# Optimization experiments

Measured on AMD Instinct MI355X. Metric: run time of the kernel, lower is better.

## Reference

```python
import jax, jax.numpy as jnp
import numpy as np

EPS = 1e-9


def _resolve(circle_pos, circle_radius, aabb_pos, aabb_half):
    Nc = circle_pos.shape[0]
    Na = aabb_pos.shape[0]

    # ---- circle vs circle: push apart along center-to-center normal ----
    d = circle_pos[:, None, :] - circle_pos[None, :, :]          # [Nc,Nc,2]
    d2 = jnp.sum(d * d, axis=-1)                                 # [Nc,Nc]
    off_diag = ~jnp.eye(Nc, dtype=bool)
    dist = jnp.sqrt(jnp.where(d2 > EPS, d2, 1.0))
    pen = circle_radius[:, None] + circle_radius[None, :] - dist
    hit = off_diag & (d2 > EPS) & (pen > 0)
    normal = d / dist[..., None]
    # each body moves half the penetration toward itself; summing over the
    # full (symmetric) matrix resolves every unordered pair exactly once
    corr_cc = jnp.sum(jnp.where(hit[..., None], 0.5 * pen[..., None] * normal, 0.0), axis=1)

    # ---- aabb vs aabb: push along minimum-overlap axis ----
    da = aabb_pos[:, None, :] - aabb_pos[None, :, :]             # [Na,Na,2]
    ov = aabb_half[:, None, :] + aabb_half[None, :, :] - jnp.abs(da)
    hit_a = (~jnp.eye(Na, dtype=bool)) & (ov[..., 0] > 0) & (ov[..., 1] > 0)
    sgn = jnp.where(da >= 0, 1.0, -1.0)
    use_x = ov[..., 0] <= ov[..., 1]
    zeros = jnp.zeros_like(ov[..., 0])
    push_x = jnp.stack([0.5 * ov[..., 0] * sgn[..., 0], zeros], axis=-1)
    push_y = jnp.stack([zeros, 0.5 * ov[..., 1] * sgn[..., 1]], axis=-1)
    push = jnp.where(use_x[..., None], push_x, push_y)
    corr_aa = jnp.sum(jnp.where(hit_a[..., None], push, 0.0), axis=1)

    # ---- circle vs aabb: closest point on box ----
    rel = circle_pos[:, None, :] - aabb_pos[None, :, :]          # [Nc,Na,2]
    closest = jnp.clip(rel, -aabb_half[None, :, :], aabb_half[None, :, :])
    diff = rel - closest
    dd2 = jnp.sum(diff * diff, axis=-1)
    ddist = jnp.sqrt(jnp.where(dd2 > EPS, dd2, 1.0))
    pen_ca = circle_radius[:, None] - ddist
    hit_ca = (dd2 > EPS) & (pen_ca > 0)
    n_ca = diff / ddist[..., None]
    push_ca = jnp.where(hit_ca[..., None], 0.5 * pen_ca[..., None] * n_ca, 0.0)
    corr_c = jnp.sum(push_ca, axis=1)     # on circles
    corr_a = -jnp.sum(push_ca, axis=0)    # equal-and-opposite on boxes

    new_circle = circle_pos + corr_cc + corr_c
    new_aabb = aabb_pos + corr_aa + corr_a
    return jnp.concatenate([new_circle, new_aabb], axis=0)   # [Nc+Na, 2]


def setup_inputs() -> dict:
    key = jax.random.key(0)
    k1, k2, k3, k4 = jax.random.split(key, 4)
    circle_pos = jax.random.normal(k1, (4096, 2), dtype=jnp.float32)
    circle_radius = jax.random.uniform(k2, (4096,), dtype=jnp.float32)
    aabb_pos = jax.random.normal(k3, (2048, 2), dtype=jnp.float32)
    aabb_half = jax.random.uniform(k4, (2048, 2), dtype=jnp.float32)
    return {"circle_pos": circle_pos, "circle_radius": circle_radius,
            "aabb_pos": aabb_pos, "aabb_half": aabb_half}


def reference(circle_pos, circle_radius, aabb_pos, aabb_half):
    return _resolve(circle_pos, circle_radius, aabb_pos, aabb_half)
```

## Files before the change

kernel.cpp:

```cpp
#include <hip/hip_runtime.h>
#include <math.h>

#define EPS 1e-9f

__global__ void prep(const float2* __restrict__ cpos,
                     const float*  __restrict__ crad,
                     const float2* __restrict__ apos,
                     const float2* __restrict__ ahalf,
                     float4* __restrict__ P,
                     float2* __restrict__ out,
                     int Nc, int Ntot) {
    int i = blockIdx.x * blockDim.x + threadIdx.x;
    if (i >= Ntot) return;
    if (i < Nc) {
        const float2 p = cpos[i];
        P[i]   = make_float4(p.x, p.y, crad[i], 0.0f);
        out[i] = p;
    } else {
        const float2 a = apos[i - Nc];
        const float2 h = ahalf[i - Nc];
        P[i]   = make_float4(a.x, a.y, h.x, h.y);
        out[i] = a;
    }
}

__global__ __launch_bounds__(256)
void collide(const float4* __restrict__ P,
             float* __restrict__ out,
             int Nc, int Ntot) {
    const int lane  = threadIdx.x & 63;
    const int w     = __builtin_amdgcn_readfirstlane(threadIdx.x >> 6);
    const int i     = (blockIdx.x << 6) + lane;
    const int jbase = (blockIdx.y * 4 + w) << 6;

    const float4 me = P[i];
    float ax = 0.0f, ay = 0.0f;

    const bool body_circle = ((int)(blockIdx.x << 6)) < Nc;
    const bool part_circle = (jbase < Nc);

    if (body_circle) {
        const float px = me.x, py = me.y, ri = me.z;
        if (part_circle) {
            #pragma unroll 8
            for (int k = 0; k < 64; ++k) {
                const float4 q = P[jbase + k];
                const float dx = px - q.x, dy = py - q.y;
                const float d2 = fmaf(dx, dx, dy * dy);
                const float r  = __builtin_amdgcn_rsqf(d2);
                const float pen = (ri + q.z) - d2 * r;
                const float s = (d2 > EPS && pen > 0.0f) ? 0.5f * pen * r : 0.0f;
                ax = fmaf(s, dx, ax);
                ay = fmaf(s, dy, ay);
            }
        } else {
            #pragma unroll 8
            for (int k = 0; k < 64; ++k) {
                const float4 q = P[jbase + k];
                const float rx = px - q.x, ry = py - q.y;
                const float cx = fminf(fmaxf(rx, -q.z), q.z);
                const float cy = fminf(fmaxf(ry, -q.w), q.w);
                const float dx = rx - cx, dy = ry - cy;
                const float d2 = fmaf(dx, dx, dy * dy);
                const float r  = __builtin_amdgcn_rsqf(d2);
                const float pen = ri - d2 * r;
                const float s = (d2 > EPS && pen > 0.0f) ? 0.5f * pen * r : 0.0f;
                ax = fmaf(s, dx, ax);
                ay = fmaf(s, dy, ay);
            }
        }
    } else {
        const float bx = me.x, by = me.y, hx = me.z, hy = me.w;
        if (part_circle) {
            #pragma unroll 8
            for (int k = 0; k < 64; ++k) {
                const float4 q = P[jbase + k];
                const float rx = q.x - bx, ry = q.y - by;
                const float cx = fminf(fmaxf(rx, -hx), hx);
                const float cy = fminf(fmaxf(ry, -hy), hy);
                const float dx = rx - cx, dy = ry - cy;
                const float d2 = fmaf(dx, dx, dy * dy);
                const float r  = __builtin_amdgcn_rsqf(d2);
                const float pen = q.z - d2 * r;
                const float s = (d2 > EPS && pen > 0.0f) ? -0.5f * pen * r : 0.0f;
                ax = fmaf(s, dx, ax);
                ay = fmaf(s, dy, ay);
            }
        } else {
            #pragma unroll 8
            for (int k = 0; k < 64; ++k) {
                const int j = jbase + k;
                const float4 q = P[j];
                const float dax = bx - q.x, day = by - q.y;
                const float ovx = hx + q.z - fabsf(dax);
                const float ovy = hy + q.w - fabsf(day);
                const bool hit = (j != i) && (ovx > 0.0f) && (ovy > 0.0f);
                const bool ux  = ovx <= ovy;
                ax += (hit && ux)  ? 0.5f * ovx * (dax >= 0.0f ? 1.0f : -1.0f) : 0.0f;
                ay += (hit && !ux) ? 0.5f * ovy * (day >= 0.0f ? 1.0f : -1.0f) : 0.0f;
            }
        }
    }

    __shared__ float sax[4][64];
    __shared__ float say[4][64];
    sax[w][lane] = ax;
    say[w][lane] = ay;
    __syncthreads();
    if (w == 0) {
        const float tx = sax[0][lane] + sax[1][lane] + sax[2][lane] + sax[3][lane];
        const float ty = say[0][lane] + say[1][lane] + say[2][lane] + say[3][lane];
        atomicAdd(&out[2 * i],     tx);
        atomicAdd(&out[2 * i + 1], ty);
    }
}

extern "C" void kernel_launch(void* const* d_in, const int* in_sizes, int n_in,
                              void* d_out, int out_size, void* d_ws, size_t ws_size,
                              hipStream_t stream) {
    (void)n_in; (void)out_size; (void)ws_size;

    const float2* cpos  = (const float2*)d_in[0];
    const float*  crad  = (const float*) d_in[1];
    const float2* apos  = (const float2*)d_in[2];
    const float2* ahalf = (const float2*)d_in[3];

    const int Nc   = in_sizes[1];
    const int Na   = in_sizes[2] / 2;
    const int Ntot = Nc + Na;

    float4* P = (float4*)d_ws;

    prep<<<(Ntot + 255) / 256, 256, 0, stream>>>(cpos, crad, apos, ahalf,
                                                 P, (float2*)d_out, Nc, Ntot);

    const int gx = (Ntot + 63) / 64;
    const int gy = (Ntot + 255) / 256;
    dim3 grid(gx, gy, 1);
    collide<<<grid, 256, 0, stream>>>(P, (float*)d_out, Nc, Ntot);
}
```

Measured before the change: 78.18 us.

## Exploit pair symmetry: process upper-triangular tile pairs with equal-and-opposite forces

```diff
diff --git a/kernel.cpp b/kernel.cpp
--- a/kernel.cpp
+++ b/kernel.cpp
@@ -14,7 +14,7 @@
     if (i >= Ntot) return;
     if (i < Nc) {
         const float2 p = cpos[i];
-        P[i]   = make_float4(p.x, p.y, crad[i], 0.0f);
+        P[i]   = make_float4(p.x, p.y, 0.5f * crad[i], 0.0f);
         out[i] = p;
     } else {
         const float2 a = apos[i - Nc];
@@ -24,95 +24,128 @@
     }
 }
 
+__device__ __forceinline__ int tri_off(int I) { return I * (193 - I) / 2; }
+
 __global__ __launch_bounds__(256)
 void collide(const float4* __restrict__ P,
              float* __restrict__ out,
-             int Nc, int Ntot) {
-    const int lane  = threadIdx.x & 63;
-    const int w     = __builtin_amdgcn_readfirstlane(threadIdx.x >> 6);
-    const int i     = (blockIdx.x << 6) + lane;
-    const int jbase = (blockIdx.y * 4 + w) << 6;
+             int Nc) {
+    const int lane = threadIdx.x & 63;
+    const int w    = threadIdx.x >> 6;
+    const int t    = blockIdx.x * 4 + w;
 
-    const float4 me = P[i];
+    int I = (int)((193.0f - sqrtf((float)(37249 - 8 * t))) * 0.5f);
+    while (tri_off(I + 1) <= t) ++I;
+    while (tri_off(I) > t) --I;
+    const int J = I + (t - tri_off(I));
+
+    const int tileC  = Nc >> 6;
+    const bool bodyC = I < tileC;
+    const bool partC = J < tileC;
+
+    __shared__ float4 Jd[4][128];
+    __shared__ float  FJx[4][128];
+    __shared__ float  FJy[4][128];
+
+    {
+        const float4 q = P[(J << 6) + lane];
+        Jd[w][lane]       = q;
+        Jd[w][lane + 64]  = q;
+        FJx[w][lane]      = 0.0f;  FJx[w][lane + 64] = 0.0f;
+        FJy[w][lane]      = 0.0f;  FJy[w][lane + 64] = 0.0f;
+    }
+    __syncthreads();
+
+    const float4 me = P[(I << 6) + lane];
     float ax = 0.0f, ay = 0.0f;
 
-    const bool body_circle = ((int)(blockIdx.x << 6)) < Nc;
-    const bool part_circle = (jbase < Nc);
-
-    if (body_circle) {
-        const float px = me.x, py = me.y, ri = me.z;
-        if (part_circle) {
+    if (I != J) {
+        if (partC) {
+            const float px = me.x, py = me.y, rih = me.z;
             #pragma unroll 8
-            for (int k = 0; k < 64; ++k) {
-                const float4 q = P[jbase + k];
-                const float dx = px - q.x, dy = py - q.y;
+            for (int m = 0; m < 64; ++m) {
+                const int slot = lane + m;
+                const float4 q = Jd[w][slot];
+                const float dx = q.x - px, dy = q.y - py;
                 const float d2 = fmaf(dx, dx, dy * dy);
                 const float r  = __builtin_amdgcn_rsqf(d2);
-                const float pen = (ri + q.z) - d2 * r;
-                const float s = (d2 > EPS && pen > 0.0f) ? 0.5f * pen * r : 0.0f;
-                ax = fmaf(s, dx, ax);
-                ay = fmaf(s, dy, ay);
+                const float s  = fmaxf(fmaf(rih + q.z, r, -0.5f), 0.0f);
+                const float fJx = s * dx, fJy = s * dy;
+                ax -= fJx; ay -= fJy;
+                atomicAdd(&FJx[w][slot], fJx);
+                atomicAdd(&FJy[w][slot], fJy);
             }
-        } else {
+        } else if (bodyC) {
+            const float px = me.x, py = me.y, rih = me.z;
             #pragma unroll 8
-            for (int k = 0; k < 64; ++k) {
-                const float4 q = P[jbase + k];
-                const float rx = px - q.x, ry = py - q.y;
+            for (int m = 0; m < 64; ++m) {
+                const int slot = lane + m;
+                const float4 q = Jd[w][slot];
+                const float rx = q.x - px, ry = q.y - py;
                 const float cx = fminf(fmaxf(rx, -q.z), q.z);
                 const float cy = fminf(fmaxf(ry, -q.w), q.w);
                 const float dx = rx - cx, dy = ry - cy;
                 const float d2 = fmaf(dx, dx, dy * dy);
                 const float r  = __builtin_amdgcn_rsqf(d2);
-                const float pen = ri - d2 * r;
-                const float s = (d2 > EPS && pen > 0.0f) ? 0.5f * pen * r : 0.0f;
-                ax = fmaf(s, dx, ax);
-                ay = fmaf(s, dy, ay);
+                float s = fmaxf(fmaf(rih, r, -0.5f), 0.0f);
+                s = (d2 > EPS) ? s : 0.0f;
+                const float fJx = s * dx, fJy = s * dy;
+                ax -= fJx; ay -= fJy;
+                atomicAdd(&FJx[w][slot], fJx);
+                atomicAdd(&FJy[w][slot], fJy);
+            }
+        } else {
+            const float bx = me.x, by = me.y, hx = me.z, hy = me.w;
+            #pragma unroll 8
+            for (int m = 0; m < 64; ++m) {
+                const int slot = lane + m;
+                const float4 q = Jd[w][slot];
+                const float dqx = q.x - bx, dqy = q.y - by;
+                const float ovx = (hx + q.z) - fabsf(dqx);
+                const float ovy = (hy + q.w) - fabsf(dqy);
+                const bool hit = fminf(ovx, ovy) > 0.0f;
+                const bool ux  = ovx <= ovy;
+                const float fJx = (hit && ux)  ? copysignf(0.5f * ovx, dqx) : 0.0f;
+                const float fJy = (hit && !ux) ? copysignf(0.5f * ovy, dqy) : 0.0f;
+                ax -= fJx; ay -= fJy;
+                atomicAdd(&FJx[w][slot], fJx);
+                atomicAdd(&FJy[w][slot], fJy);
             }
         }
+        const float gx = FJx[w][lane] + FJx[w][lane + 64];
+        const float gy = FJy[w][lane] + FJy[w][lane + 64];
+        atomicAdd(&out[(((J << 6) + lane) << 1)],     gx);
+        atomicAdd(&out[(((J << 6) + lane) << 1) + 1], gy);
     } else {
-        const float bx = me.x, by = me.y, hx = me.z, hy = me.w;
-        if (part_circle) {
-            #pragma unroll 8
-            for (int k = 0; k < 64; ++k) {
-                const float4 q = P[jbase + k];
-                const float rx = q.x - bx, ry = q.y - by;
-                const float cx = fminf(fmaxf(rx, -hx), hx);
-                const float cy = fminf(fmaxf(ry, -hy), hy);
-                const float dx = rx - cx, dy = ry - cy;
+        if (bodyC) {
+            const float px = me.x, py = me.y, rih = me.z;
+            #pragma unroll 7
+            for (int k = 1; k < 64; ++k) {
+                const float4 q = Jd[w][lane + k];
+                const float dx = px - q.x, dy = py - q.y;
                 const float d2 = fmaf(dx, dx, dy * dy);
                 const float r  = __builtin_amdgcn_rsqf(d2);
-                const float pen = q.z - d2 * r;
-                const float s = (d2 > EPS && pen > 0.0f) ? -0.5f * pen * r : 0.0f;
-                ax = fmaf(s, dx, ax);
-                ay = fmaf(s, dy, ay);
+                const float s  = fmaxf(fmaf(rih + q.z, r, -0.5f), 0.0f);
+                ax = fmaf(s, dx, ax); ay = fmaf(s, dy, ay);
             }
         } else {
-            #pragma unroll 8
-            for (int k = 0; k < 64; ++k) {
-                const int j = jbase + k;
-                const float4 q = P[j];
+            const float bx = me.x, by = me.y, hx = me.z, hy = me.w;
+            #pragma unroll 7
+            for (int k = 1; k < 64; ++k) {
+                const float4 q = Jd[w][lane + k];
                 const float dax = bx - q.x, day = by - q.y;
-                const float ovx = hx + q.z - fabsf(dax);
-                const float ovy = hy + q.w - fabsf(day);
-                const bool hit = (j != i) && (ovx > 0.0f) && (ovy > 0.0f);
+                const float ovx = (hx + q.z) - fabsf(dax);
+                const float ovy = (hy + q.w) - fabsf(day);
+                const bool hit = fminf(ovx, ovy) > 0.0f;
                 const bool ux  = ovx <= ovy;
-                ax += (hit && ux)  ? 0.5f * ovx * (dax >= 0.0f ? 1.0f : -1.0f) : 0.0f;
-                ay += (hit && !ux) ? 0.5f * ovy * (day >= 0.0f ? 1.0f : -1.0f) : 0.0f;
+                ax += (hit && ux)  ? copysignf(0.5f * ovx, dax) : 0.0f;
+                ay += (hit && !ux) ? copysignf(0.5f * ovy, day) : 0.0f;
             }
         }
     }
 
-    __shared__ float sax[4][64];
-    __shared__ float say[4][64];
-    sax[w][lane] = ax;
-    say[w][lane] = ay;
-    __syncthreads();
-    if (w == 0) {
-        const float tx = sax[0][lane] + sax[1][lane] + sax[2][lane] + sax[3][lane];
-        const float ty = say[0][lane] + say[1][lane] + say[2][lane] + say[3][lane];
-        atomicAdd(&out[2 * i],     tx);
-        atomicAdd(&out[2 * i + 1], ty);
-    }
+    atomicAdd(&out[(((I << 6) + lane) << 1)],     ax);
+    atomicAdd(&out[(((I << 6) + lane) << 1) + 1], ay);
 }
 
 extern "C" void kernel_launch(void* const* d_in, const int* in_sizes, int n_in,
@@ -134,8 +167,7 @@
     prep<<<(Ntot + 255) / 256, 256, 0, stream>>>(cpos, crad, apos, ahalf,
                                                  P, (float2*)d_out, Nc, Ntot);
 
-    const int gx = (Ntot + 63) / 64;
-    const int gy = (Ntot + 255) / 256;
-    dim3 grid(gx, gy, 1);
-    collide<<<grid, 256, 0, stream>>>(P, (float*)d_out, Nc, Ntot);
+    const int tile_pairs = (96 * 97) / 2;
+    const int blocks = tile_pairs / 4;
+    collide<<<blocks, 256, 0, stream>>>(P, (float*)d_out, Nc);
 }
```

Result: slower. 271.4 us (+247.1%).
